# Kernel optimization log

Hardware: AMD Instinct MI355X
Metric: run time of the kernel (lower is better)

## Reference

```python
import jax, jax.numpy as jnp
import numpy as np

M = 50000   # eval points
N = 1024    # gaussians
EPS = 1e-6


def setup_inputs() -> dict:
    key = jax.random.key(0)
    k1, k2, k3 = jax.random.split(key, 3)
    points = jax.random.uniform(k1, (M, 3), dtype=jnp.float32)          # normalized coords in [0,1)
    positions = jax.random.uniform(k2, (N, 3), dtype=jnp.float32)       # torch.rand init
    log_scales = jnp.full((N, 3), -3.0, dtype=jnp.float32)              # torch.full(..., -3.0)
    intensities = jax.random.uniform(k3, (N,), dtype=jnp.float32) * 0.5  # torch.rand * 0.5
    return {"points": points, "positions": positions,
            "log_scales": log_scales, "intensities": intensities}


def reference(points, positions, log_scales, intensities):
    # Faithful translation of FastGaussianModel._eval_gaussians
    scales = jnp.exp(log_scales)                      # [N,3]
    inv_var = 1.0 / (scales ** 2 + EPS)               # [N,3]
    diff = points[:, None, :] - positions[None, :, :] # [M,N,3]
    quad = jnp.einsum('mnd,nd->mn', diff * diff, inv_var)  # [M,N]
    gauss = jnp.exp(-0.5 * quad)                      # [M,N]
    values = gauss @ intensities                      # [M]
    return values
```

## Files before the change

kernel.cpp:

```cpp
#include <hip/hip_runtime.h>


constexpr int NG_CHUNK = 128;
constexpr int BLOCK    = 256;

__global__ void fgm_prep(const float* __restrict__ positions,
                         const float* __restrict__ log_scales,
                         const float* __restrict__ intensities,
                         float* __restrict__ coef, int N, int Npad) {
    int n = blockIdx.x * blockDim.x + threadIdx.x;
    if (n >= Npad) return;
    float4 c0 = make_float4(0.f, 0.f, 0.f, 0.f);
    float4 c1 = make_float4(0.f, 0.f, 0.f, 0.f);
    if (n < N) {
        const float K = -0.7213475204444817f;
        float q0 = positions[3*n+0], q1 = positions[3*n+1], q2 = positions[3*n+2];
        float iv0 = 1.0f / (__expf(2.0f*log_scales[3*n+0]) + 1e-6f);
        float iv1 = 1.0f / (__expf(2.0f*log_scales[3*n+1]) + 1e-6f);
        float iv2 = 1.0f / (__expf(2.0f*log_scales[3*n+2]) + 1e-6f);
        float c = iv0*q0*q0 + iv1*q1*q1 + iv2*q2*q2;
        c0 = make_float4(K*(-2.f*iv0*q0), K*(-2.f*iv1*q1), K*(-2.f*iv2*q2), K*iv0);
        c1 = make_float4(K*iv1, K*iv2, K*c, intensities[n]);
    }
    float4* out = (float4*)coef;
    out[2*n+0] = c0;
    out[2*n+1] = c1;
}

__global__ __launch_bounds__(BLOCK) void fgm_main(const float* __restrict__ points,
                                                  const float* __restrict__ coef,
                                                  float* __restrict__ out, int M) {
    __shared__ float4 sc[NG_CHUNK * 2];
    int base = blockIdx.y * NG_CHUNK;
    const float4* gc = (const float4*)coef + base * 2;
    sc[threadIdx.x] = gc[threadIdx.x];
    __syncthreads();

    int m = blockIdx.x * blockDim.x + threadIdx.x;
    float px = 0.f, py = 0.f, pz = 0.f;
    if (m < M) {
        px = points[3*m+0];
        py = points[3*m+1];
        pz = points[3*m+2];
    }
    float px2 = px*px, py2 = py*py, pz2 = pz*pz;
    float acc = 0.f;
    #pragma unroll 4
    for (int n = 0; n < NG_CHUNK; ++n) {
        float4 c0 = sc[2*n+0];
        float4 c1 = sc[2*n+1];
        float t = __builtin_fmaf(c0.x, px,  c1.z);
        t = __builtin_fmaf(c0.y, py,  t);
        t = __builtin_fmaf(c0.z, pz,  t);
        t = __builtin_fmaf(c0.w, px2, t);
        t = __builtin_fmaf(c1.x, py2, t);
        t = __builtin_fmaf(c1.y, pz2, t);
        float g = __builtin_amdgcn_exp2f(t);
        acc = __builtin_fmaf(g, c1.w, acc);
    }
    if (m < M) atomicAdd(&out[m], acc);
}

extern "C" void kernel_launch(void* const* d_in, const int* in_sizes, int n_in,
                              void* d_out, int out_size, void* d_ws, size_t ws_size,
                              hipStream_t stream) {
    const float* points      = (const float*)d_in[0];
    const float* positions   = (const float*)d_in[1];
    const float* log_scales  = (const float*)d_in[2];
    const float* intensities = (const float*)d_in[3];
    int M = in_sizes[0] / 3;
    int N = in_sizes[3];

    int chunks = (N + NG_CHUNK - 1) / NG_CHUNK;
    int Npad   = chunks * NG_CHUNK;

    float* coef = (float*)d_ws;

    hipMemsetAsync(d_out, 0, (size_t)out_size * sizeof(float), stream);

    fgm_prep<<<(Npad + 255) / 256, 256, 0, stream>>>(positions, log_scales,
                                                     intensities, coef, N, Npad);

    dim3 grid((M + BLOCK - 1) / BLOCK, chunks);
    fgm_main<<<grid, BLOCK, 0, stream>>>(points, coef, (float*)d_out, M);
}
```

Measured before the change: 76.40 us.

## Use SoA coefficients with packed float2 FMAs and drop LDS staging

The prep kernel now writes the coefficients in a structure-of-arrays layout. The main kernel reads them directly from global memory as float2 pairs, which are uniform across the block and can become scalar or broadcast loads, so the LDS staging and the barrier are removed. The quadratic-form evaluation processes two Gaussians at a time with packed v2f FMAs, which can map to v_pk_fma_f32 on CDNA3/4, halving the FMA instruction count. The exp2 calls stay scalar, and the loop depends on the compiler emitting scalar or cached loads instead of per-thread global loads.

```diff
diff --git a/kernel.cpp b/kernel.cpp
--- a/kernel.cpp
+++ b/kernel.cpp
@@ -1,5 +1,7 @@
 #include <hip/hip_runtime.h>
 
+
+typedef float v2f __attribute__((ext_vector_type(2)));
 
 constexpr int NG_CHUNK = 128;
 constexpr int BLOCK    = 256;
@@ -10,32 +12,28 @@
                          float* __restrict__ coef, int N, int Npad) {
     int n = blockIdx.x * blockDim.x + threadIdx.x;
     if (n >= Npad) return;
-    float4 c0 = make_float4(0.f, 0.f, 0.f, 0.f);
-    float4 c1 = make_float4(0.f, 0.f, 0.f, 0.f);
+    float a0=0.f, a1=0.f, a2=0.f, b0=0.f, b1=0.f, b2=0.f, c=0.f, w=0.f;
     if (n < N) {
         const float K = -0.7213475204444817f;
         float q0 = positions[3*n+0], q1 = positions[3*n+1], q2 = positions[3*n+2];
         float iv0 = 1.0f / (__expf(2.0f*log_scales[3*n+0]) + 1e-6f);
         float iv1 = 1.0f / (__expf(2.0f*log_scales[3*n+1]) + 1e-6f);
         float iv2 = 1.0f / (__expf(2.0f*log_scales[3*n+2]) + 1e-6f);
-        float c = iv0*q0*q0 + iv1*q1*q1 + iv2*q2*q2;
-        c0 = make_float4(K*(-2.f*iv0*q0), K*(-2.f*iv1*q1), K*(-2.f*iv2*q2), K*iv0);
-        c1 = make_float4(K*iv1, K*iv2, K*c, intensities[n]);
+        a0 = K * (-2.f*iv0*q0);  b0 = K * iv0;
+        a1 = K * (-2.f*iv1*q1);  b1 = K * iv1;
+        a2 = K * (-2.f*iv2*q2);  b2 = K * iv2;
+        c  = K * (iv0*q0*q0 + iv1*q1*q1 + iv2*q2*q2);
+        w  = intensities[n];
     }
-    float4* out = (float4*)coef;
-    out[2*n+0] = c0;
-    out[2*n+1] = c1;
+    coef[0*Npad+n] = a0;  coef[1*Npad+n] = a1;  coef[2*Npad+n] = a2;
+    coef[3*Npad+n] = b0;  coef[4*Npad+n] = b1;  coef[5*Npad+n] = b2;
+    coef[6*Npad+n] = c;   coef[7*Npad+n] = w;
 }
 
 __global__ __launch_bounds__(BLOCK) void fgm_main(const float* __restrict__ points,
                                                   const float* __restrict__ coef,
-                                                  float* __restrict__ out, int M) {
-    __shared__ float4 sc[NG_CHUNK * 2];
-    int base = blockIdx.y * NG_CHUNK;
-    const float4* gc = (const float4*)coef + base * 2;
-    sc[threadIdx.x] = gc[threadIdx.x];
-    __syncthreads();
-
+                                                  float* __restrict__ out,
+                                                  int M, int Npad) {
     int m = blockIdx.x * blockDim.x + threadIdx.x;
     float px = 0.f, py = 0.f, pz = 0.f;
     if (m < M) {
@@ -43,22 +41,34 @@
         py = points[3*m+1];
         pz = points[3*m+2];
     }
-    float px2 = px*px, py2 = py*py, pz2 = pz*pz;
-    float acc = 0.f;
+    v2f vpx  = {px, px},       vpy  = {py, py},       vpz  = {pz, pz};
+    v2f vpx2 = {px*px, px*px}, vpy2 = {py*py, py*py}, vpz2 = {pz*pz, pz*pz};
+
+    int half = blockIdx.y * (NG_CHUNK/2);
+    const v2f* A0 = (const v2f*)(coef + 0*Npad) + half;
+    const v2f* A1 = (const v2f*)(coef + 1*Npad) + half;
+    const v2f* A2 = (const v2f*)(coef + 2*Npad) + half;
+    const v2f* B0 = (const v2f*)(coef + 3*Npad) + half;
+    const v2f* B1 = (const v2f*)(coef + 4*Npad) + half;
+    const v2f* B2 = (const v2f*)(coef + 5*Npad) + half;
+    const v2f* C  = (const v2f*)(coef + 6*Npad) + half;
+    const v2f* W  = (const v2f*)(coef + 7*Npad) + half;
+
+    v2f acc = {0.f, 0.f};
     #pragma unroll 4
-    for (int n = 0; n < NG_CHUNK; ++n) {
-        float4 c0 = sc[2*n+0];
-        float4 c1 = sc[2*n+1];
-        float t = __builtin_fmaf(c0.x, px,  c1.z);
-        t = __builtin_fmaf(c0.y, py,  t);
-        t = __builtin_fmaf(c0.z, pz,  t);
-        t = __builtin_fmaf(c0.w, px2, t);
-        t = __builtin_fmaf(c1.x, py2, t);
-        t = __builtin_fmaf(c1.y, pz2, t);
-        float g = __builtin_amdgcn_exp2f(t);
-        acc = __builtin_fmaf(g, c1.w, acc);
+    for (int i = 0; i < NG_CHUNK/2; ++i) {
+        v2f t = __builtin_elementwise_fma(A0[i], vpx,  C[i]);
+        t = __builtin_elementwise_fma(A1[i], vpy,  t);
+        t = __builtin_elementwise_fma(A2[i], vpz,  t);
+        t = __builtin_elementwise_fma(B0[i], vpx2, t);
+        t = __builtin_elementwise_fma(B1[i], vpy2, t);
+        t = __builtin_elementwise_fma(B2[i], vpz2, t);
+        v2f g;
+        g.x = __builtin_amdgcn_exp2f(t.x);
+        g.y = __builtin_amdgcn_exp2f(t.y);
+        acc = __builtin_elementwise_fma(g, W[i], acc);
     }
-    if (m < M) atomicAdd(&out[m], acc);
+    if (m < M) atomicAdd(&out[m], acc.x + acc.y);
 }
 
 extern "C" void kernel_launch(void* const* d_in, const int* in_sizes, int n_in,
@@ -82,5 +92,5 @@
                                                      intensities, coef, N, Npad);
 
     dim3 grid((M + BLOCK - 1) / BLOCK, chunks);
-    fgm_main<<<grid, BLOCK, 0, stream>>>(points, coef, (float*)d_out, M);
+    fgm_main<<<grid, BLOCK, 0, stream>>>(points, coef, (float*)d_out, M, Npad);
 }
```

After: 77.07 us. No clear change (+0.9%).

## Bin gaussians and points into spatial grid and cull distant cells

Applied to the files above, without the earlier changes.

Sorts gaussians and evaluation points into an 8x8x8 cell grid, then each block computes its points' bounding box and skips gaussian cells whose minimum exponent is below a cutoff. When all gaussians share one scale, a cheaper per-gaussian formula is used with the point-dependent term precomputed. This removes most of the dense M×N exp work at the cost of extra histogram, scan and sort launches, a single-block scatter, and a truncation error from the cutoff. A full dense fallback path handles non-uniform scales.

```diff
diff --git a/kernel.cpp b/kernel.cpp
--- a/kernel.cpp
+++ b/kernel.cpp
@@ -1,64 +1,226 @@
 #include <hip/hip_runtime.h>
 
 
-constexpr int NG_CHUNK = 128;
-constexpr int BLOCK    = 256;
-
-__global__ void fgm_prep(const float* __restrict__ positions,
-                         const float* __restrict__ log_scales,
-                         const float* __restrict__ intensities,
-                         float* __restrict__ coef, int N, int Npad) {
-    int n = blockIdx.x * blockDim.x + threadIdx.x;
-    if (n >= Npad) return;
-    float4 c0 = make_float4(0.f, 0.f, 0.f, 0.f);
-    float4 c1 = make_float4(0.f, 0.f, 0.f, 0.f);
-    if (n < N) {
-        const float K = -0.7213475204444817f;
+constexpr int   CELLS  = 512;
+constexpr int   GRID1D = 8;
+constexpr float CELLH  = 0.125f;
+constexpr int   NSLICE = 16;
+constexpr int   BLOCK  = 128;
+constexpr float TCUT   = -20.0f;
+
+__device__ __forceinline__ int cell_of(float x, float y, float z) {
+    int cx = min(GRID1D - 1, max(0, (int)(x * GRID1D)));
+    int cy = min(GRID1D - 1, max(0, (int)(y * GRID1D)));
+    int cz = min(GRID1D - 1, max(0, (int)(z * GRID1D)));
+    return (cx << 6) | (cy << 3) | cz;
+}
+
+__global__ void fgm_zero(float* __restrict__ out, int out_n,
+                         int* __restrict__ hists ) {
+    int i = blockIdx.x * blockDim.x + threadIdx.x;
+    int stride = gridDim.x * blockDim.x;
+    for (int k = i; k < out_n; k += stride) out[k] = 0.f;
+    for (int k = i; k < 2 * CELLS; k += stride) hists[k] = 0;
+}
+
+__global__ void fgm_hist(const float* __restrict__ points,
+                         const float* __restrict__ positions,
+                         int M, int N,
+                         int* __restrict__ ghist, int* __restrict__ phist) {
+    int i = blockIdx.x * blockDim.x + threadIdx.x;
+    int stride = gridDim.x * blockDim.x;
+    for (int n = i; n < N; n += stride) {
+        int c = cell_of(positions[3*n], positions[3*n+1], positions[3*n+2]);
+        atomicAdd(&ghist[c], 1);
+    }
+    for (int m = i; m < M; m += stride) {
+        int c = cell_of(points[3*m], points[3*m+1], points[3*m+2]);
+        atomicAdd(&phist[c], 1);
+    }
+}
+
+__global__ void fgm_scan_scatter(const float* __restrict__ positions,
+                                 const float* __restrict__ log_scales,
+                                 const float* __restrict__ intensities,
+                                 float* __restrict__ ws,
+                                 const int* __restrict__ ghist,
+                                 const int* __restrict__ phist,
+                                 int* __restrict__ gStart,
+                                 int* __restrict__ pofs,
+                                 float* __restrict__ fastT,
+                                 float* __restrict__ fullT,
+                                 int N) {
+    __shared__ int sa[CELLS], sb[CELLS], gofs[CELLS];
+    __shared__ int smism;
+    int t = threadIdx.x;
+    if (t == 0) smism = 0;
+
+    sa[t] = ghist[t];
+    __syncthreads();
+    int* src = sa; int* dst = sb;
+    for (int off = 1; off < CELLS; off <<= 1) {
+        int v = src[t];
+        if (t >= off) v += src[t - off];
+        dst[t] = v;
+        __syncthreads();
+        int* tmp = src; src = dst; dst = tmp;
+    }
+    int ginc = src[t];
+    gStart[t + 1] = ginc;
+    if (t == 0) gStart[0] = 0;
+    gofs[t] = ginc - ghist[t];
+    __syncthreads();
+
+    sa[t] = phist[t];
+    __syncthreads();
+    src = sa; dst = sb;
+    for (int off = 1; off < CELLS; off <<= 1) {
+        int v = src[t];
+        if (t >= off) v += src[t - off];
+        dst[t] = v;
+        __syncthreads();
+        int* tmp = src; src = dst; dst = tmp;
+    }
+    pofs[t] = src[t] - phist[t];
+    __syncthreads();
+
+    const float K = -0.7213475204444817f;
+    float r0 = K / (__expf(2.0f*log_scales[0]) + 1e-6f);
+    float r1 = K / (__expf(2.0f*log_scales[1]) + 1e-6f);
+    float r2 = K / (__expf(2.0f*log_scales[2]) + 1e-6f);
+
+    int mism = 0;
+    for (int n = t; n < N; n += blockDim.x) {
         float q0 = positions[3*n+0], q1 = positions[3*n+1], q2 = positions[3*n+2];
-        float iv0 = 1.0f / (__expf(2.0f*log_scales[3*n+0]) + 1e-6f);
-        float iv1 = 1.0f / (__expf(2.0f*log_scales[3*n+1]) + 1e-6f);
-        float iv2 = 1.0f / (__expf(2.0f*log_scales[3*n+2]) + 1e-6f);
-        float c = iv0*q0*q0 + iv1*q1*q1 + iv2*q2*q2;
-        c0 = make_float4(K*(-2.f*iv0*q0), K*(-2.f*iv1*q1), K*(-2.f*iv2*q2), K*iv0);
-        c1 = make_float4(K*iv1, K*iv2, K*c, intensities[n]);
-    }
-    float4* out = (float4*)coef;
-    out[2*n+0] = c0;
-    out[2*n+1] = c1;
-}
-
-__global__ __launch_bounds__(BLOCK) void fgm_main(const float* __restrict__ points,
-                                                  const float* __restrict__ coef,
-                                                  float* __restrict__ out, int M) {
-    __shared__ float4 sc[NG_CHUNK * 2];
-    int base = blockIdx.y * NG_CHUNK;
-    const float4* gc = (const float4*)coef + base * 2;
-    sc[threadIdx.x] = gc[threadIdx.x];
-    __syncthreads();
-
-    int m = blockIdx.x * blockDim.x + threadIdx.x;
+        float b0 = K / (__expf(2.0f*log_scales[3*n+0]) + 1e-6f);
+        float b1 = K / (__expf(2.0f*log_scales[3*n+1]) + 1e-6f);
+        float b2 = K / (__expf(2.0f*log_scales[3*n+2]) + 1e-6f);
+        float a0 = -2.f*b0*q0, a1 = -2.f*b1*q1, a2 = -2.f*b2*q2;
+        float c  = b0*q0*q0 + b1*q1*q1 + b2*q2*q2;
+        float w  = intensities[n];
+        if (b0 != r0 || b1 != r1 || b2 != r2) mism = 1;
+        int cell = cell_of(q0, q1, q2);
+        int slot = atomicAdd(&gofs[cell], 1);
+        float4* f = (float4*)(fastT + (size_t)slot * 8);
+        f[0] = make_float4(a0, a1, a2, c);
+        f[1] = make_float4(w, 0.f, 0.f, 0.f);
+        float4* o = (float4*)(fullT + (size_t)slot * 8);
+        o[0] = make_float4(a0, a1, a2, b0);
+        o[1] = make_float4(b1, b2, c, w);
+    }
+    if (mism) atomicOr(&smism, 1);
+    __syncthreads();
+    if (t == 0) {
+        ws[0] = smism ? 1.f : 0.f;
+        ws[1] = r0;  ws[2] = r1;  ws[3] = r2;
+    }
+}
+
+__global__ void fgm_psort(const float* __restrict__ points, int M,
+                          int* __restrict__ pofs,
+                          float4* __restrict__ sortedPts) {
+    int i = blockIdx.x * blockDim.x + threadIdx.x;
+    int stride = gridDim.x * blockDim.x;
+    for (int m = i; m < M; m += stride) {
+        float x = points[3*m], y = points[3*m+1], z = points[3*m+2];
+        int c = cell_of(x, y, z);
+        int slot = atomicAdd(&pofs[c], 1);
+        sortedPts[slot] = make_float4(x, y, z, __int_as_float(m));
+    }
+}
+
+__global__ __launch_bounds__(BLOCK) void fgm_main(const float4* __restrict__ sortedPts,
+                                                  const float* __restrict__ ws,
+                                                  const int* __restrict__ gStart,
+                                                  const float* __restrict__ fastT,
+                                                  const float* __restrict__ fullT,
+                                                  float* __restrict__ out,
+                                                  int M, int N) {
+    __shared__ float sbb[2][6];
+
+    int tid  = threadIdx.x;
+    int lane = tid & 63;
+    int wave = tid >> 6;
+    int i = blockIdx.x * BLOCK + tid;
+
+    bool fast = (ws[0] == 0.f);
+    float r0 = ws[1], r1 = ws[2], r2 = ws[3];
+
     float px = 0.f, py = 0.f, pz = 0.f;
-    if (m < M) {
-        px = points[3*m+0];
-        py = points[3*m+1];
-        pz = points[3*m+2];
-    }
-    float px2 = px*px, py2 = py*py, pz2 = pz*pz;
+    int morig = -1;
+    if (i < M) {
+        float4 pr = sortedPts[i];
+        px = pr.x; py = pr.y; pz = pr.z;
+        morig = __float_as_int(pr.w);
+    }
+    float pp = r0*px*px + r1*py*py + r2*pz*pz;
     float acc = 0.f;
-    #pragma unroll 4
-    for (int n = 0; n < NG_CHUNK; ++n) {
-        float4 c0 = sc[2*n+0];
-        float4 c1 = sc[2*n+1];
-        float t = __builtin_fmaf(c0.x, px,  c1.z);
-        t = __builtin_fmaf(c0.y, py,  t);
-        t = __builtin_fmaf(c0.z, pz,  t);
-        t = __builtin_fmaf(c0.w, px2, t);
-        t = __builtin_fmaf(c1.x, py2, t);
-        t = __builtin_fmaf(c1.y, pz2, t);
-        float g = __builtin_amdgcn_exp2f(t);
-        acc = __builtin_fmaf(g, c1.w, acc);
-    }
-    if (m < M) atomicAdd(&out[m], acc);
+
+    if (fast) {
+        float lox = px, loy = py, loz = pz, hix = px, hiy = py, hiz = pz;
+        if (i >= M) {
+            lox = loy = loz =  1e30f;
+            hix = hiy = hiz = -1e30f;
+        }
+        #pragma unroll
+        for (int off = 32; off >= 1; off >>= 1) {
+            lox = fminf(lox, __shfl_xor(lox, off));
+            loy = fminf(loy, __shfl_xor(loy, off));
+            loz = fminf(loz, __shfl_xor(loz, off));
+            hix = fmaxf(hix, __shfl_xor(hix, off));
+            hiy = fmaxf(hiy, __shfl_xor(hiy, off));
+            hiz = fmaxf(hiz, __shfl_xor(hiz, off));
+        }
+        if (lane == 0) {
+            sbb[wave][0] = lox; sbb[wave][1] = loy; sbb[wave][2] = loz;
+            sbb[wave][3] = hix; sbb[wave][4] = hiy; sbb[wave][5] = hiz;
+        }
+        __syncthreads();
+        lox = fminf(sbb[0][0], sbb[1][0]);
+        loy = fminf(sbb[0][1], sbb[1][1]);
+        loz = fminf(sbb[0][2], sbb[1][2]);
+        hix = fmaxf(sbb[0][3], sbb[1][3]);
+        hiy = fmaxf(sbb[0][4], sbb[1][4]);
+        hiz = fmaxf(sbb[0][5], sbb[1][5]);
+
+        for (int c = blockIdx.y; c < CELLS; c += NSLICE) {
+            int gLo = gStart[c], gHi = gStart[c + 1];
+            if (gLo == gHi) continue;
+            int cx = c >> 6, cy = (c >> 3) & 7, cz = c & 7;
+            float cxl = cx * CELLH, cyl = cy * CELLH, czl = cz * CELLH;
+            float dx = fmaxf(0.f, fmaxf(cxl - hix, lox - (cxl + CELLH)));
+            float dy = fmaxf(0.f, fmaxf(cyl - hiy, loy - (cyl + CELLH)));
+            float dz = fmaxf(0.f, fmaxf(czl - hiz, loz - (czl + CELLH)));
+            float tmax = r0*dx*dx + r1*dy*dy + r2*dz*dz;
+            if (tmax < TCUT) continue;
+            for (int g = gLo; g < gHi; ++g) {
+                const float4* rp = (const float4*)(fastT + (size_t)g * 8);
+                float4 rA = rp[0];
+                float4 rB = rp[1];
+                float t = rA.w + pp;
+                t = __builtin_fmaf(rA.z, pz, t);
+                t = __builtin_fmaf(rA.y, py, t);
+                t = __builtin_fmaf(rA.x, px, t);
+                acc = __builtin_fmaf(__builtin_amdgcn_exp2f(t), rB.x, acc);
+            }
+        }
+    } else {
+        float qx = px*px, qy = py*py, qz = pz*pz;
+        for (int g = blockIdx.y; g < N; g += NSLICE) {
+            const float4* rp = (const float4*)(fullT + (size_t)g * 8);
+            float4 rA = rp[0];
+            float4 rB = rp[1];
+            float t = __builtin_fmaf(rA.w, qx, rB.z);
+            t = __builtin_fmaf(rB.x, qy, t);
+            t = __builtin_fmaf(rB.y, qz, t);
+            t = __builtin_fmaf(rA.z, pz, t);
+            t = __builtin_fmaf(rA.y, py, t);
+            t = __builtin_fmaf(rA.x, px, t);
+            acc = __builtin_fmaf(__builtin_amdgcn_exp2f(t), rB.w, acc);
+        }
+    }
+
+    if (i < M) atomicAdd(&out[morig], acc);
 }
 
 extern "C" void kernel_launch(void* const* d_in, const int* in_sizes, int n_in,
@@ -71,16 +233,29 @@
     int M = in_sizes[0] / 3;
     int N = in_sizes[3];
 
-    int chunks = (N + NG_CHUNK - 1) / NG_CHUNK;
-    int Npad   = chunks * NG_CHUNK;
-
-    float* coef = (float*)d_ws;
-
-    hipMemsetAsync(d_out, 0, (size_t)out_size * sizeof(float), stream);
-
-    fgm_prep<<<(Npad + 255) / 256, 256, 0, stream>>>(positions, log_scales,
-                                                     intensities, coef, N, Npad);
-
-    dim3 grid((M + BLOCK - 1) / BLOCK, chunks);
-    fgm_main<<<grid, BLOCK, 0, stream>>>(points, coef, (float*)d_out, M);
-}
+    float* ws  = (float*)d_ws;
+    int*   wsi = (int*)d_ws;
+    int* ghist  = wsi + 16;
+    int* phist  = wsi + 528;
+    int* gStart = wsi + 1040;
+    int* pofs   = wsi + 1553;
+    float4* sortedPts = (float4*)(ws + 2080);
+    float*  fastT     = ws + 2080 + (size_t)4 * M;
+    float*  fullT     = fastT + (size_t)8 * N;
+
+    int zb = (max(out_size, 2 * CELLS) + 255) / 256;
+    fgm_zero<<<zb, 256, 0, stream>>>((float*)d_out, out_size, ghist);
+
+    int hb = (max(M, N) + 255) / 256;
+    fgm_hist<<<hb, 256, 0, stream>>>(points, positions, M, N, ghist, phist);
+
+    fgm_scan_scatter<<<1, CELLS, 0, stream>>>(positions, log_scales, intensities,
+                                              ws, ghist, phist, gStart, pofs,
+                                              fastT, fullT, N);
+
+    fgm_psort<<<(M + 255) / 256, 256, 0, stream>>>(points, M, pofs, sortedPts);
+
+    dim3 grid((M + BLOCK - 1) / BLOCK, NSLICE);
+    fgm_main<<<grid, BLOCK, 0, stream>>>(sortedPts, ws, gStart, fastT, fullT,
+                                         (float*)d_out, M, N);
+}
```

After: 157.8 us. +106.5%, slower.
